# Performance work log

Hardware: AMD Instinct MI355X
Metric: run time of the kernel (lower is better)

## Reference

```python
import jax, jax.numpy as jnp
import numpy as np

N_NODES = 50000
N_EDGES = 600000
D = 128
EDGE_VOCAB = 10


def setup_inputs() -> dict:
    key = jax.random.key(0)
    ks = jax.random.split(key, 8)
    x = jax.random.normal(ks[0], (N_NODES, D), dtype=jnp.float32)
    edge_index = jax.random.randint(ks[1], (2, N_EDGES), 0, N_NODES, dtype=jnp.int64)
    edge_weight = jax.random.randint(ks[2], (N_EDGES,), 0, EDGE_VOCAB, dtype=jnp.int64)
    cat_list = jax.random.randint(ks[3], (N_NODES,), 0, 4, dtype=jnp.int64)
    # edge embedding initialized uniform [0,1) as in torch.nn.init.uniform_
    edge_emb = jax.random.uniform(ks[4], (EDGE_VOCAB, D), dtype=jnp.float32)
    # nn.Linear default init ~ U(-1/sqrt(in), 1/sqrt(in))
    lim = 1.0 / np.sqrt(D)
    W_l = jax.random.uniform(ks[5], (D, D), minval=-lim, maxval=lim, dtype=jnp.float32)
    b_l = jax.random.uniform(ks[6], (D,), minval=-lim, maxval=lim, dtype=jnp.float32)
    W_r = jax.random.uniform(ks[7], (D, D), minval=-lim, maxval=lim, dtype=jnp.float32)
    b_r = jax.random.uniform(jax.random.fold_in(key, 99), (D,), minval=-lim, maxval=lim, dtype=jnp.float32)
    return {"x": x, "edge_emb": edge_emb, "W_l": W_l, "b_l": b_l,
            "W_r": W_r, "b_r": b_r, "edge_index": edge_index,
            "edge_weight": edge_weight, "cat_list": cat_list}


def reference(x, edge_emb, W_l, b_l, W_r, b_r, edge_index, edge_weight, cat_list):
    # Active H_GAT path: real_GNN(x, edge_index, edge_weight)
    src = edge_index[0]  # x_j (source nodes, PyG source_to_target flow)
    dst = edge_index[1]  # aggregation index
    # message: edge embedding lookup * gathered neighbor features  [E, D]
    msg = edge_emb[edge_weight] * x[src]
    # aggregate: scatter-sum to destination nodes  [N, D]
    prop = jax.ops.segment_sum(msg, dst, num_segments=x.shape[0])
    # out = lin_l(x) + lin_r(prop)
    out = x @ W_l.T + b_l + prop @ W_r.T + b_r
    return out
```

## Files before the change

kernel.cpp:

```cpp
#include <hip/hip_runtime.h>

#define N_NODES 50000
#define N_EDGES 600000
#define D 128
#define SCAN_BLOCKS ((N_NODES + 255) / 256)

typedef __attribute__((ext_vector_type(8))) short short8v;
typedef __attribute__((ext_vector_type(4))) float f32x4;

__device__ __forceinline__ unsigned short f2bf(float v) {
    unsigned u = __builtin_bit_cast(unsigned, v);
    u += 0x7FFFu + ((u >> 16) & 1u);
    return (unsigned short)(u >> 16);
}
__device__ __forceinline__ float bf2f(unsigned short h) {
    unsigned u = ((unsigned)h) << 16;
    return __builtin_bit_cast(float, u);
}

#define XPREP_BLOCKS ((N_NODES * D / 8 + 255) / 256)
__global__ __launch_bounds__(256) void prep_kernel(
    const float* __restrict__ Wl, const float* __restrict__ Wr,
    unsigned short* __restrict__ Bh, unsigned short* __restrict__ Bl,
    const float* __restrict__ x, unsigned short* __restrict__ xbf,
    int* __restrict__ counts)
{
    int bid = blockIdx.x;
    if (bid < 128) {
        int t = bid * 256 + threadIdx.x;
        int n = t >> 8;
        int k = t & 255;
        float w = (k < 128) ? Wl[n * 128 + k] : Wr[n * 128 + (k - 128)];
        unsigned short h = f2bf(w);
        Bh[t] = h;
        Bl[t] = f2bf(w - bf2f(h));
    } else if (bid < 128 + XPREP_BLOCKS) {
        int t = (bid - 128) * 256 + threadIdx.x;
        if (t < N_NODES * D / 8) {
            const float4* p = (const float4*)(x + (size_t)t * 8);
            float4 a = p[0], b = p[1];
            short8v o;
            o[0] = (short)f2bf(a.x); o[1] = (short)f2bf(a.y);
            o[2] = (short)f2bf(a.z); o[3] = (short)f2bf(a.w);
            o[4] = (short)f2bf(b.x); o[5] = (short)f2bf(b.y);
            o[6] = (short)f2bf(b.z); o[7] = (short)f2bf(b.w);
            *(short8v*)(xbf + (size_t)t * 8) = o;
        }
    } else {
        int t = (bid - 128 - XPREP_BLOCKS) * 256 + threadIdx.x;
        if (t < N_NODES) counts[t] = 0;
    }
}


__global__ __launch_bounds__(256) void histrank_kernel(
    const int* __restrict__ ei, int* __restrict__ counts,
    int* __restrict__ rank)
{
    int e = blockIdx.x * blockDim.x + threadIdx.x;
    if (e >= N_EDGES) return;
    rank[e] = atomicAdd(&counts[ei[N_EDGES + e]], 1);
}

__global__ __launch_bounds__(256) void scan_phase1(
    const int* __restrict__ counts, int* __restrict__ blockSums)
{
    int i = blockIdx.x * 256 + threadIdx.x;
    int v = (i < N_NODES) ? counts[i] : 0;
#pragma unroll
    for (int off = 32; off > 0; off >>= 1) v += __shfl_down(v, off, 64);
    __shared__ int wsum[4];
    int lane = threadIdx.x & 63, wid = threadIdx.x >> 6;
    if (lane == 0) wsum[wid] = v;
    __syncthreads();
    if (threadIdx.x == 0)
        blockSums[blockIdx.x] = wsum[0] + wsum[1] + wsum[2] + wsum[3];
}

__global__ __launch_bounds__(256) void scan_phase2(
    const int* __restrict__ blockSums, int* __restrict__ blockOffs,
    int* __restrict__ offs)
{
    __shared__ int sh[256];
    int t = threadIdx.x;
    int v = (t < SCAN_BLOCKS) ? blockSums[t] : 0;
    sh[t] = v;
    __syncthreads();
    for (int off = 1; off < 256; off <<= 1) {
        int u = (t >= off) ? sh[t - off] : 0;
        __syncthreads();
        sh[t] += u;
        __syncthreads();
    }
    if (t < SCAN_BLOCKS) blockOffs[t] = sh[t] - v;
    if (t == 0) offs[N_NODES] = N_EDGES;
}

__global__ __launch_bounds__(256) void scan_phase3(
    const int* __restrict__ counts,
    const int* __restrict__ blockOffs,
    int* __restrict__ offs)
{
    int t = threadIdx.x;
    int i = blockIdx.x * 256 + t;
    int v = (i < N_NODES) ? counts[i] : 0;
    int lane = t & 63, wid = t >> 6;
    int s = v;
#pragma unroll
    for (int off = 1; off < 64; off <<= 1) {
        int u = __shfl_up(s, off, 64);
        if (lane >= off) s += u;
    }
    __shared__ int wsum[4];
    if (lane == 63) wsum[wid] = s;
    __syncthreads();
    int wadd = 0;
    for (int w = 0; w < wid; w++) wadd += wsum[w];
    if (i < N_NODES)
        offs[i] = blockOffs[blockIdx.x] + s + wadd - v;
}

__global__ __launch_bounds__(256) void pack_kernel(
    const int* __restrict__ ei,
    const int* __restrict__ ew,
    const int* __restrict__ offs,
    const int* __restrict__ rank,
    unsigned* __restrict__ packed)
{
    int e = blockIdx.x * blockDim.x + threadIdx.x;
    if (e >= N_EDGES) return;
    int dst = ei[N_EDGES + e];
    int r   = rank[e];
    int pos = offs[dst] + r;
    packed[pos] = (unsigned)ei[e] | ((unsigned)ew[e] << 16);
}

__global__ __launch_bounds__(256) void aggregate_kernel(
    const unsigned short* __restrict__ xbf,
    const float* __restrict__ emb,
    const int* __restrict__ offs,
    const unsigned* __restrict__ packed,
    float* __restrict__ prop)
{
    __shared__ float emb_s[10][D];
    for (int i = threadIdx.x; i < 10 * D; i += 256)
        emb_s[i >> 7][i & 127] = emb[i];
    __syncthreads();

    int node = blockIdx.x * 4 + (threadIdx.x >> 6);
    if (node >= N_NODES) return;
    int c = (threadIdx.x & 63) * 2;

    int beg = offs[node], end = offs[node + 1];
    float2 acc = make_float2(0.f, 0.f);

    for (int i = beg; i < end; i += 16) {
        unsigned pk[16];
#pragma unroll
        for (int q = 0; q < 16; q++) {
            int j = i + q;
            j = (j < end) ? j : end - 1;
            pk[q] = packed[j];
        }
        unsigned xr[16];
#pragma unroll
        for (int q = 0; q < 16; q++)
            xr[q] = *(const unsigned*)(xbf + (size_t)(pk[q] & 0xFFFFu) * D + c);
#pragma unroll
        for (int q = 0; q < 16; q++) {
            float s = (i + q < end) ? 1.f : 0.f;
            const float* er = &emb_s[pk[q] >> 16][c];
            acc.x += s * er[0] * bf2f((unsigned short)(xr[q] & 0xFFFFu));
            acc.y += s * er[1] * bf2f((unsigned short)(xr[q] >> 16));
        }
    }
    *(float2*)(prop + (size_t)node * D + c) = acc;
}


__global__ void zero_kernel(float4* __restrict__ out, int n4) {
    int i = blockIdx.x * blockDim.x + threadIdx.x;
    int stride = gridDim.x * blockDim.x;
    for (; i < n4; i += stride) out[i] = make_float4(0.f, 0.f, 0.f, 0.f);
}

__global__ __launch_bounds__(256) void scatter_kernel(
    const float* __restrict__ x,
    const float* __restrict__ emb,
    const int*   __restrict__ ei,
    const int*   __restrict__ ew,
    float*       __restrict__ prop)
{
    int gid = blockIdx.x * blockDim.x + threadIdx.x;
    int e = gid >> 5;
    if (e >= N_EDGES) return;
    int d4 = (gid & 31) * 4;
    int src = ei[e];
    int dst = ei[N_EDGES + e];
    int w   = ew[e];
    float4 ev = *(const float4*)(emb + (size_t)w * D + d4);
    float4 xv = *(const float4*)(x + (size_t)src * D + d4);
    float* p = prop + (size_t)dst * D + d4;
    atomicAdd(p + 0, ev.x * xv.x);
    atomicAdd(p + 1, ev.y * xv.y);
    atomicAdd(p + 2, ev.z * xv.z);
    atomicAdd(p + 3, ev.w * xv.w);
}


__global__ __launch_bounds__(256) void mfma_gemm(
    const float* __restrict__ x,
    float*       __restrict__ out,
    const unsigned short* __restrict__ Bh,
    const unsigned short* __restrict__ Bl,
    const float* __restrict__ bl_,
    const float* __restrict__ br_)
{
    __shared__ unsigned short Ah_s[128 * 40];
    __shared__ unsigned short Al_s[128 * 40];
    __shared__ unsigned short Bh_s[128 * 40];
    __shared__ unsigned short Bl_s[128 * 40];

    const int tid  = threadIdx.x;
    const int lane = tid & 63;
    const int wave = tid >> 6;
    const int row0 = blockIdx.x * 128;

    const int wr0 = (wave >> 1) * 64;
    const int wc0 = (wave & 1) * 64;
    const int lr  = lane & 15;
    const int lk8 = (lane >> 4) * 8;

    const int srow  = tid >> 1;
    const int skoff = (tid & 1) * 16;

    f32x4 acc[4][4];
#pragma unroll
    for (int i = 0; i < 4; i++)
#pragma unroll
        for (int j = 0; j < 4; j++)
            acc[i][j] = (f32x4){0.f, 0.f, 0.f, 0.f};

    for (int kc = 0; kc < 8; ++kc) {
        const int kbase = kc * 32;
        {
            const float* Asrc = (kbase < 128) ? x : out;
            const int acol = (kbase & 127) + skoff;
            const int grow = row0 + srow;
            float v[16];
            if (grow < N_NODES) {
                const float4* p = (const float4*)(Asrc + (size_t)grow * D + acol);
#pragma unroll
                for (int q = 0; q < 4; q++) {
                    float4 f = p[q];
                    v[q*4+0] = f.x; v[q*4+1] = f.y; v[q*4+2] = f.z; v[q*4+3] = f.w;
                }
            } else {
#pragma unroll
                for (int q = 0; q < 16; q++) v[q] = 0.f;
            }
            short8v h0, h1, l0, l1;
#pragma unroll
            for (int q = 0; q < 8; q++) {
                unsigned short h = f2bf(v[q]);
                h0[q] = (short)h;
                l0[q] = (short)f2bf(v[q] - bf2f(h));
            }
#pragma unroll
            for (int q = 0; q < 8; q++) {
                unsigned short h = f2bf(v[q + 8]);
                h1[q] = (short)h;
                l1[q] = (short)f2bf(v[q + 8] - bf2f(h));
            }
            *(short8v*)(Ah_s + srow * 40 + skoff)     = h0;
            *(short8v*)(Ah_s + srow * 40 + skoff + 8) = h1;
            *(short8v*)(Al_s + srow * 40 + skoff)     = l0;
            *(short8v*)(Al_s + srow * 40 + skoff + 8) = l1;
        }
        {
            const size_t boff = (size_t)srow * 256 + kbase + skoff;
            short8v bh0 = *(const short8v*)(Bh + boff);
            short8v bh1 = *(const short8v*)(Bh + boff + 8);
            short8v bl0 = *(const short8v*)(Bl + boff);
            short8v bl1 = *(const short8v*)(Bl + boff + 8);
            *(short8v*)(Bh_s + srow * 40 + skoff)     = bh0;
            *(short8v*)(Bh_s + srow * 40 + skoff + 8) = bh1;
            *(short8v*)(Bl_s + srow * 40 + skoff)     = bl0;
            *(short8v*)(Bl_s + srow * 40 + skoff + 8) = bl1;
        }
        __syncthreads();
        short8v afh[4], afl[4];
#pragma unroll
        for (int rt = 0; rt < 4; rt++) {
            int ar = wr0 + rt * 16 + lr;
            afh[rt] = *(const short8v*)(Ah_s + ar * 40 + lk8);
            afl[rt] = *(const short8v*)(Al_s + ar * 40 + lk8);
        }
#pragma unroll
        for (int ct = 0; ct < 4; ct++) {
            int bc = wc0 + ct * 16 + lr;
            short8v bfh = *(const short8v*)(Bh_s + bc * 40 + lk8);
            short8v bfl = *(const short8v*)(Bl_s + bc * 40 + lk8);
#pragma unroll
            for (int rt = 0; rt < 4; rt++)
                acc[rt][ct] = __builtin_amdgcn_mfma_f32_16x16x32_bf16(afh[rt], bfh, acc[rt][ct], 0, 0, 0);
#pragma unroll
            for (int rt = 0; rt < 4; rt++)
                acc[rt][ct] = __builtin_amdgcn_mfma_f32_16x16x32_bf16(afl[rt], bfh, acc[rt][ct], 0, 0, 0);
#pragma unroll
            for (int rt = 0; rt < 4; rt++)
                acc[rt][ct] = __builtin_amdgcn_mfma_f32_16x16x32_bf16(afh[rt], bfl, acc[rt][ct], 0, 0, 0);
        }
        __syncthreads();
    }

    const int drow = (lane >> 4) * 4;
#pragma unroll
    for (int ct = 0; ct < 4; ct++) {
        int col = wc0 + ct * 16 + lr;
        float bias = bl_[col] + br_[col];
#pragma unroll
        for (int rt = 0; rt < 4; rt++) {
#pragma unroll
            for (int r = 0; r < 4; r++) {
                int grow = row0 + wr0 + rt * 16 + drow + r;
                if (grow < N_NODES)
                    out[(size_t)grow * D + col] = acc[rt][ct][r] + bias;
            }
        }
    }
}

extern "C" void kernel_launch(void* const* d_in, const int* in_sizes, int n_in,
                              void* d_out, int out_size, void* d_ws, size_t ws_size,
                              hipStream_t stream) {
    const float* x    = (const float*)d_in[0];
    const float* emb  = (const float*)d_in[1];
    const float* W_l  = (const float*)d_in[2];
    const float* b_l  = (const float*)d_in[3];
    const float* W_r  = (const float*)d_in[4];
    const float* b_r  = (const float*)d_in[5];
    const int*   ei   = (const int*)d_in[6];
    const int*   ew   = (const int*)d_in[7];

    float* out = (float*)d_out;

    char* wsp = (char*)d_ws;
    unsigned short* Bh  = (unsigned short*)wsp; wsp += 128 * 256 * sizeof(unsigned short);
    unsigned short* Bl  = (unsigned short*)wsp; wsp += 128 * 256 * sizeof(unsigned short);
    unsigned short* xbf = (unsigned short*)wsp; wsp += (size_t)N_NODES * D * sizeof(unsigned short);
    int*      counts    = (int*)wsp;     wsp += N_NODES * sizeof(int);
    int*      offs      = (int*)wsp;     wsp += (N_NODES + 1) * sizeof(int);
    int*      rank      = (int*)wsp;     wsp += N_EDGES * sizeof(int);
    int*      blockSums = (int*)wsp;     wsp += SCAN_BLOCKS * sizeof(int);
    int*      blockOffs = (int*)wsp;     wsp += SCAN_BLOCKS * sizeof(int);
    unsigned* packed    = (unsigned*)wsp; wsp += N_EDGES * sizeof(unsigned);
    size_t needed = (size_t)(wsp - (char*)d_ws);

    if (ws_size >= needed) {
        prep_kernel<<<128 + XPREP_BLOCKS + SCAN_BLOCKS, 256, 0, stream>>>(
            W_l, W_r, Bh, Bl, x, xbf, counts);
        histrank_kernel<<<(N_EDGES + 255) / 256, 256, 0, stream>>>(ei, counts, rank);
        scan_phase1<<<SCAN_BLOCKS, 256, 0, stream>>>(counts, blockSums);
        scan_phase2<<<1, 256, 0, stream>>>(blockSums, blockOffs, offs);
        scan_phase3<<<SCAN_BLOCKS, 256, 0, stream>>>(counts, blockOffs, offs);
        pack_kernel<<<(N_EDGES + 255) / 256, 256, 0, stream>>>(ei, ew, offs, rank, packed);
        aggregate_kernel<<<(N_NODES + 3) / 4, 256, 0, stream>>>(xbf, emb, offs, packed, out);
        mfma_gemm<<<(N_NODES + 127) / 128, 256, 0, stream>>>(x, out, Bh, Bl, b_l, b_r);
    } else {
        prep_kernel<<<128, 256, 0, stream>>>(W_l, W_r, Bh, Bl, x, xbf, counts);
        int n4 = N_NODES * D / 4;
        zero_kernel<<<(n4 + 255) / 256, 256, 0, stream>>>((float4*)out, n4);
        long long work = (long long)N_EDGES * 32;
        scatter_kernel<<<(int)((work + 255) / 256), 256, 0, stream>>>(x, emb, ei, ew, out);
        mfma_gemm<<<(N_NODES + 127) / 128, 256, 0, stream>>>(x, out, Bh, Bl, b_l, b_r);
    }
}
```

Baseline: 115.1 us.

## Pad CSR segments to 16 with sentinel edges and widen aggregate vector loads

Each node's edge list is rounded up to a multiple of 16 and the padded slots are filled with a sentinel source index that points at a zeroed extra xbf row. This lets the aggregate kernel drop per-edge masking and load packed entries as aligned uint4. The aggregate kernel now uses 32 lanes per node with 4 columns each, so loads are wider and more nodes fit per block. The cost is a packed buffer more than twice as large that has to be sentinel-filled every call, plus extra padded gather work on the zero row.

```diff
diff --git a/kernel.cpp b/kernel.cpp
--- a/kernel.cpp
+++ b/kernel.cpp
@@ -4,6 +4,9 @@
 #define N_EDGES 600000
 #define D 128
 #define SCAN_BLOCKS ((N_NODES + 255) / 256)
+#define PACK_CAP 1351680
+#define PFILL_BLOCKS (PACK_CAP / 1024)
+#define SENTINEL 50000u
 
 typedef __attribute__((ext_vector_type(8))) short short8v;
 typedef __attribute__((ext_vector_type(4))) float f32x4;
@@ -23,7 +26,7 @@
     const float* __restrict__ Wl, const float* __restrict__ Wr,
     unsigned short* __restrict__ Bh, unsigned short* __restrict__ Bl,
     const float* __restrict__ x, unsigned short* __restrict__ xbf,
-    int* __restrict__ counts)
+    int* __restrict__ counts, unsigned* __restrict__ packed)
 {
     int bid = blockIdx.x;
     if (bid < 128) {
@@ -46,9 +49,18 @@
             o[6] = (short)f2bf(b.z); o[7] = (short)f2bf(b.w);
             *(short8v*)(xbf + (size_t)t * 8) = o;
         }
-    } else {
+    } else if (bid < 128 + XPREP_BLOCKS + SCAN_BLOCKS) {
         int t = (bid - 128 - XPREP_BLOCKS) * 256 + threadIdx.x;
         if (t < N_NODES) counts[t] = 0;
+    } else if (bid < 128 + XPREP_BLOCKS + SCAN_BLOCKS + PFILL_BLOCKS) {
+        int t = (bid - 128 - XPREP_BLOCKS - SCAN_BLOCKS) * 1024 + threadIdx.x * 4;
+        uint4 s = make_uint4(SENTINEL, SENTINEL, SENTINEL, SENTINEL);
+        *(uint4*)(packed + t) = s;
+    } else {
+        if (threadIdx.x < 16) {
+            short8v z = (short8v){0,0,0,0,0,0,0,0};
+            *(short8v*)(xbf + (size_t)N_NODES * D + threadIdx.x * 8) = z;
+        }
     }
 }
 
@@ -66,7 +78,7 @@
     const int* __restrict__ counts, int* __restrict__ blockSums)
 {
     int i = blockIdx.x * 256 + threadIdx.x;
-    int v = (i < N_NODES) ? counts[i] : 0;
+    int v = (i < N_NODES) ? ((counts[i] + 15) & ~15) : 0;
 #pragma unroll
     for (int off = 32; off > 0; off >>= 1) v += __shfl_down(v, off, 64);
     __shared__ int wsum[4];
@@ -93,7 +105,7 @@
         __syncthreads();
     }
     if (t < SCAN_BLOCKS) blockOffs[t] = sh[t] - v;
-    if (t == 0) offs[N_NODES] = N_EDGES;
+    if (t == 255) offs[N_NODES] = sh[255];
 }
 
 __global__ __launch_bounds__(256) void scan_phase3(
@@ -103,7 +115,7 @@
 {
     int t = threadIdx.x;
     int i = blockIdx.x * 256 + t;
-    int v = (i < N_NODES) ? counts[i] : 0;
+    int v = (i < N_NODES) ? ((counts[i] + 15) & ~15) : 0;
     int lane = t & 63, wid = t >> 6;
     int s = v;
 #pragma unroll
@@ -147,34 +159,39 @@
         emb_s[i >> 7][i & 127] = emb[i];
     __syncthreads();
 
-    int node = blockIdx.x * 4 + (threadIdx.x >> 6);
+    int node = blockIdx.x * 8 + (threadIdx.x >> 5);
     if (node >= N_NODES) return;
-    int c = (threadIdx.x & 63) * 2;
+    int c = (threadIdx.x & 31) * 4;
 
     int beg = offs[node], end = offs[node + 1];
-    float2 acc = make_float2(0.f, 0.f);
-
-    for (int i = beg; i < end; i += 16) {
+    float4 acc = make_float4(0.f, 0.f, 0.f, 0.f);
+
+    for (int i = beg; __any(i < end); i += 16) {
+        int ib = (i < end) ? i : (PACK_CAP - 16);
+        uint4 pk4[4];
+#pragma unroll
+        for (int qq = 0; qq < 4; qq++)
+            pk4[qq] = *(const uint4*)(packed + ib + qq * 4);
         unsigned pk[16];
 #pragma unroll
+        for (int qq = 0; qq < 4; qq++) {
+            pk[qq*4+0] = pk4[qq].x; pk[qq*4+1] = pk4[qq].y;
+            pk[qq*4+2] = pk4[qq].z; pk[qq*4+3] = pk4[qq].w;
+        }
+        uint2 xr[16];
+#pragma unroll
+        for (int q = 0; q < 16; q++)
+            xr[q] = *(const uint2*)(xbf + (size_t)(pk[q] & 0xFFFFu) * D + c);
+#pragma unroll
         for (int q = 0; q < 16; q++) {
-            int j = i + q;
-            j = (j < end) ? j : end - 1;
-            pk[q] = packed[j];
-        }
-        unsigned xr[16];
-#pragma unroll
-        for (int q = 0; q < 16; q++)
-            xr[q] = *(const unsigned*)(xbf + (size_t)(pk[q] & 0xFFFFu) * D + c);
-#pragma unroll
-        for (int q = 0; q < 16; q++) {
-            float s = (i + q < end) ? 1.f : 0.f;
-            const float* er = &emb_s[pk[q] >> 16][c];
-            acc.x += s * er[0] * bf2f((unsigned short)(xr[q] & 0xFFFFu));
-            acc.y += s * er[1] * bf2f((unsigned short)(xr[q] >> 16));
-        }
-    }
-    *(float2*)(prop + (size_t)node * D + c) = acc;
+            float4 er = *(const float4*)&emb_s[pk[q] >> 16][c];
+            acc.x += er.x * bf2f((unsigned short)(xr[q].x & 0xFFFFu));
+            acc.y += er.y * bf2f((unsigned short)(xr[q].x >> 16));
+            acc.z += er.z * bf2f((unsigned short)(xr[q].y & 0xFFFFu));
+            acc.w += er.w * bf2f((unsigned short)(xr[q].y >> 16));
+        }
+    }
+    *(float4*)(prop + (size_t)node * D + c) = acc;
 }
 
 
@@ -348,27 +365,27 @@
     char* wsp = (char*)d_ws;
     unsigned short* Bh  = (unsigned short*)wsp; wsp += 128 * 256 * sizeof(unsigned short);
     unsigned short* Bl  = (unsigned short*)wsp; wsp += 128 * 256 * sizeof(unsigned short);
-    unsigned short* xbf = (unsigned short*)wsp; wsp += (size_t)N_NODES * D * sizeof(unsigned short);
+    unsigned short* xbf = (unsigned short*)wsp; wsp += (size_t)(N_NODES + 1) * D * sizeof(unsigned short);
     int*      counts    = (int*)wsp;     wsp += N_NODES * sizeof(int);
     int*      offs      = (int*)wsp;     wsp += (N_NODES + 1) * sizeof(int);
     int*      rank      = (int*)wsp;     wsp += N_EDGES * sizeof(int);
     int*      blockSums = (int*)wsp;     wsp += SCAN_BLOCKS * sizeof(int);
     int*      blockOffs = (int*)wsp;     wsp += SCAN_BLOCKS * sizeof(int);
-    unsigned* packed    = (unsigned*)wsp; wsp += N_EDGES * sizeof(unsigned);
+    unsigned* packed    = (unsigned*)wsp; wsp += (size_t)PACK_CAP * sizeof(unsigned);
     size_t needed = (size_t)(wsp - (char*)d_ws);
 
     if (ws_size >= needed) {
-        prep_kernel<<<128 + XPREP_BLOCKS + SCAN_BLOCKS, 256, 0, stream>>>(
-            W_l, W_r, Bh, Bl, x, xbf, counts);
+        prep_kernel<<<128 + XPREP_BLOCKS + SCAN_BLOCKS + PFILL_BLOCKS + 1, 256, 0, stream>>>(
+            W_l, W_r, Bh, Bl, x, xbf, counts, packed);
         histrank_kernel<<<(N_EDGES + 255) / 256, 256, 0, stream>>>(ei, counts, rank);
         scan_phase1<<<SCAN_BLOCKS, 256, 0, stream>>>(counts, blockSums);
         scan_phase2<<<1, 256, 0, stream>>>(blockSums, blockOffs, offs);
         scan_phase3<<<SCAN_BLOCKS, 256, 0, stream>>>(counts, blockOffs, offs);
         pack_kernel<<<(N_EDGES + 255) / 256, 256, 0, stream>>>(ei, ew, offs, rank, packed);
-        aggregate_kernel<<<(N_NODES + 3) / 4, 256, 0, stream>>>(xbf, emb, offs, packed, out);
+        aggregate_kernel<<<(N_NODES + 7) / 8, 256, 0, stream>>>(xbf, emb, offs, packed, out);
         mfma_gemm<<<(N_NODES + 127) / 128, 256, 0, stream>>>(x, out, Bh, Bl, b_l, b_r);
     } else {
-        prep_kernel<<<128, 256, 0, stream>>>(W_l, W_r, Bh, Bl, x, xbf, counts);
+        prep_kernel<<<128, 256, 0, stream>>>(W_l, W_r, Bh, Bl, x, xbf, counts, packed);
         int n4 = N_NODES * D / 4;
         zero_kernel<<<(n4 + 255) / 256, 256, 0, stream>>>((float4*)out, n4);
         long long work = (long long)N_EDGES * 32;
```

Result: faster. 106.7 us (-7.3%).
